# Kernel tuning notes

Measured on AMD Instinct MI355X. Metric: run time of the kernel, lower is better.

Reference implementation:

```python
import jax, jax.numpy as jnp
import numpy as np

INPUT_DIM = 8
TIMESTEPS = 4096
BATCH = 1024


def setup_inputs() -> dict:
    key = jax.random.key(0)
    k1, k2, k3 = jax.random.split(key, 3)
    x = jax.random.normal(k1, (BATCH, TIMESTEPS, INPUT_DIM), dtype=jnp.float32)
    # sklearn MinMaxScaler attributes; keep scale_ bounded away from zero
    min_ = jax.random.uniform(k2, (INPUT_DIM,), dtype=jnp.float32)
    scale_ = jax.random.uniform(k3, (INPUT_DIM,), dtype=jnp.float32) * 0.9 + 0.1
    return {"x": x, "min_": min_, "scale_": scale_}


def reference(x, min_, scale_):
    D = x.shape[-1]
    # inverse MinMax transform: (x - min_) / scale_ per feature column
    x_inv = (x.reshape(-1, D) - min_) / scale_  # (N, D), N = B*T

    device_and_status = x_inv[:, 2]    # (N,)
    activity_and_status = x_inv[:, 3]  # (N,)

    in_range = (device_and_status >= 0.0) & (device_and_status <= 252.0)
    device_and_status_penalty = jnp.sum(jnp.where(in_range, 0.0, 1.0))

    is_out_of_range = (activity_and_status < 0.0) | (activity_and_status > 22.0)
    activity_and_status_penalty = jnp.sum(is_out_of_range.astype(jnp.float32))

    # sequential transition scan, vectorized: the while_loop body is a pure
    # function of (a[i-1], a[i]) with a scalar branch -> shifted compare.
    prev = activity_and_status[:-1]
    cur = activity_and_status[1:]
    cond = (jnp.mod(prev, 2.0) == 0.0) & (prev < 20.0)
    invalid = (cur != prev + 1.0) & (cur != 22.0)
    invalid_transition_penalty = jnp.sum(
        jnp.where(cond, invalid.astype(jnp.float32), 0.0)
    )

    num_activities = jnp.sum((activity_and_status != 22.0).astype(jnp.float32))
    activity_count_penalty = jnp.abs(num_activities - 58.0)

    return (device_and_status_penalty + activity_and_status_penalty
            + invalid_transition_penalty + activity_count_penalty)
```

## Files before the change

kernel.cpp:

```cpp
#include <hip/hip_runtime.h>
#include <math.h>

#define NROWS  (1024 * 4096)
#define E      (NROWS * 2)
#define BLOCKS 2048
#define TPB    256
#define RP     16
#define NW     (TPB / 64)

__global__ __launch_bounds__(TPB) void penalty_main(
        const float* __restrict__ x,
        const float* __restrict__ min_,
        const float* __restrict__ scale_,
        unsigned int* __restrict__ part) {
    const float min2 = min_[2], min3 = min_[3];
    const float sc2  = scale_[2], sc3 = scale_[3];

    const int tid  = threadIdx.x;
    const int lane = tid & 63;
    const int wave = tid >> 6;
    const unsigned G = BLOCKS * TPB;
    const unsigned t = blockIdx.x * TPB + tid;
    const bool even = ((t & 1u) == 0u);

    const float4* __restrict__ x4 = (const float4*)x;
    float4 v[RP];
    #pragma unroll
    for (int r = 0; r < RP; ++r) v[r] = x4[t + (unsigned)r * G];
    asm volatile("" ::: "memory");

    float a[RP];
    unsigned c1 = 0, c2 = 0, c4 = 0;
    #pragma unroll
    for (int r = 0; r < RP; ++r) {
        const float d = (v[r].z - min2) / sc2;
        a[r] = (v[r].w - min3) / sc3;
        if (even) {
            c1 += !(d >= 0.0f && d <= 252.0f);
            c2 += (a[r] < 0.0f) || (a[r] > 22.0f);
            c4 += (a[r] != 22.0f);
        }
    }

    __shared__ float sA[NW][RP];
    if (lane == 0) {
        #pragma unroll
        for (int r = 0; r < RP; ++r) sA[wave][r] = a[r];
    }
    __syncthreads();

    float abound[RP];
    if (tid == TPB - 2) {
        #pragma unroll
        for (int r = 0; r < RP; ++r) {
            const unsigned idx2 = t + (unsigned)r * G + 2u;
            abound[r] = (idx2 < (unsigned)E)
                      ? (x[4u * idx2 + 3u] - min3) / sc3 : 0.0f;
        }
    }

    unsigned c3 = 0;
    #pragma unroll
    for (int r = 0; r < RP; ++r) {
        float an = __shfl_down(a[r], 2);
        if (lane == 62) an = (wave < NW - 1) ? sA[wave + 1][r] : abound[r];
        if (even) {
            const unsigned idx = t + (unsigned)r * G;
            const bool cond = (fmodf(a[r], 2.0f) == 0.0f) && (a[r] < 20.0f)
                              && (idx + 2u < (unsigned)E);
            const bool invalid = (an != a[r] + 1.0f) && (an != 22.0f);
            c3 += (cond && invalid);
        }
    }

    for (int off = 32; off > 0; off >>= 1) {
        c1 += __shfl_down(c1, off);
        c2 += __shfl_down(c2, off);
        c3 += __shfl_down(c3, off);
        c4 += __shfl_down(c4, off);
    }
    __shared__ unsigned int s[NW][4];
    if (lane == 0) { s[wave][0] = c1; s[wave][1] = c2; s[wave][2] = c3; s[wave][3] = c4; }
    __syncthreads();
    if (tid == 0) {
        unsigned t1 = 0, t2 = 0, t3 = 0, t4 = 0;
        #pragma unroll
        for (int w = 0; w < NW; ++w) {
            t1 += s[w][0]; t2 += s[w][1]; t3 += s[w][2]; t4 += s[w][3];
        }
        unsigned int* p = part + 4u * blockIdx.x;
        p[0] = t1; p[1] = t2; p[2] = t3; p[3] = t4;
    }
}

__global__ __launch_bounds__(TPB) void finalize(
        const unsigned int* __restrict__ part, float* __restrict__ out) {
    const int tid = threadIdx.x;
    unsigned c1 = 0, c2 = 0, c3 = 0, c4 = 0;
    for (int b = tid; b < BLOCKS; b += TPB) {
        const unsigned int* p = part + 4 * b;
        c1 += p[0]; c2 += p[1]; c3 += p[2]; c4 += p[3];
    }
    for (int off = 32; off > 0; off >>= 1) {
        c1 += __shfl_down(c1, off);
        c2 += __shfl_down(c2, off);
        c3 += __shfl_down(c3, off);
        c4 += __shfl_down(c4, off);
    }
    __shared__ unsigned int s[NW][4];
    const int lane = tid & 63, wave = tid >> 6;
    if (lane == 0) { s[wave][0] = c1; s[wave][1] = c2; s[wave][2] = c3; s[wave][3] = c4; }
    __syncthreads();
    if (tid == 0) {
        unsigned t1 = 0, t2 = 0, t3 = 0, t4 = 0;
        #pragma unroll
        for (int w = 0; w < NW; ++w) {
            t1 += s[w][0]; t2 += s[w][1]; t3 += s[w][2]; t4 += s[w][3];
        }
        out[0] = (float)t1 + (float)t2 + (float)t3
               + fabsf((float)t4 - 58.0f);
    }
}

extern "C" void kernel_launch(void* const* d_in, const int* in_sizes, int n_in,
                              void* d_out, int out_size, void* d_ws, size_t ws_size,
                              hipStream_t stream) {
    const float* x  = (const float*)d_in[0];
    const float* mn = (const float*)d_in[1];
    const float* sc = (const float*)d_in[2];
    unsigned int* part = (unsigned int*)d_ws;
    float* out = (float*)d_out;

    penalty_main<<<BLOCKS, TPB, 0, stream>>>(x, mn, sc, part);
    finalize<<<1, TPB, 0, stream>>>(part, out);
}
```

Measured before the change: 210.5 us.

## Issue batched global loads via inline asm and halve rows per thread

Replaces the compiler-generated float4 loads with eight explicit global_load_dwordx4 instructions in inline assembly, using SGPR base plus VGPR offset and a single waitcnt, so all loads are in flight together. Rows per thread drop from sixteen to eight and the block count doubles to keep coverage the same. The intent is tighter memory-level parallelism, lower register pressure and higher occupancy for this bandwidth-bound reduction. In exchange there are fewer bytes in flight per thread, and the inline asm relies on 32-bit offsets being correct.

Result: no change. 208.6 us (-0.9%).

```diff
diff --git a/kernel.cpp b/kernel.cpp
--- a/kernel.cpp
+++ b/kernel.cpp
@@ -3,10 +3,12 @@
 
 #define NROWS  (1024 * 4096)
 #define E      (NROWS * 2)
-#define BLOCKS 2048
+#define BLOCKS 4096
 #define TPB    256
-#define RP     16
+#define RP     8
 #define NW     (TPB / 64)
+
+typedef float vf4 __attribute__((ext_vector_type(4)));
 
 __global__ __launch_bounds__(TPB) void penalty_main(
         const float* __restrict__ x,
@@ -23,11 +25,34 @@
     const unsigned t = blockIdx.x * TPB + tid;
     const bool even = ((t & 1u) == 0u);
 
-    const float4* __restrict__ x4 = (const float4*)x;
-    float4 v[RP];
-    #pragma unroll
-    for (int r = 0; r < RP; ++r) v[r] = x4[t + (unsigned)r * G];
-    asm volatile("" ::: "memory");
+    unsigned o0 = t * 16u;
+    unsigned o1 = o0 + 1u * (G * 16u);
+    unsigned o2 = o0 + 2u * (G * 16u);
+    unsigned o3 = o0 + 3u * (G * 16u);
+    unsigned o4 = o0 + 4u * (G * 16u);
+    unsigned o5 = o0 + 5u * (G * 16u);
+    unsigned o6 = o0 + 6u * (G * 16u);
+    unsigned o7 = o0 + 7u * (G * 16u);
+
+    vf4 v0, v1, v2, v3, v4, v5, v6, v7;
+    asm volatile(
+        "global_load_dwordx4 %0, %8,  %16\n\t"
+        "global_load_dwordx4 %1, %9,  %16\n\t"
+        "global_load_dwordx4 %2, %10, %16\n\t"
+        "global_load_dwordx4 %3, %11, %16\n\t"
+        "global_load_dwordx4 %4, %12, %16\n\t"
+        "global_load_dwordx4 %5, %13, %16\n\t"
+        "global_load_dwordx4 %6, %14, %16\n\t"
+        "global_load_dwordx4 %7, %15, %16\n\t"
+        "s_waitcnt vmcnt(0)"
+        : "=v"(v0), "=v"(v1), "=v"(v2), "=v"(v3),
+          "=v"(v4), "=v"(v5), "=v"(v6), "=v"(v7)
+        : "v"(o0), "v"(o1), "v"(o2), "v"(o3),
+          "v"(o4), "v"(o5), "v"(o6), "v"(o7),
+          "s"(x)
+        : "memory");
+
+    vf4 v[RP] = {v0, v1, v2, v3, v4, v5, v6, v7};
 
     float a[RP];
     unsigned c1 = 0, c2 = 0, c4 = 0;
```
